# Kernel optimization log

Measured on AMD Instinct MI355X. Metric: run time of the kernel, lower is better.

Reference implementation:

```python
import jax, jax.numpy as jnp
import numpy as np
from jax import lax

B, S, F, H, O, U = 512, 168, 12, 128, 3, 256
PERIODS = (3, 6, 12, 24)


def _glorot(key, shape):
    fan_in = shape[-1]
    fan_out = shape[-2] if len(shape) >= 2 else shape[-1]
    scale = jnp.sqrt(2.0 / (fan_in + fan_out))
    return jax.random.normal(key, shape, jnp.float32) * scale


def setup_inputs() -> dict:
    key = jax.random.key(0)
    ks = iter(jax.random.split(key, 64))
    inp = {"x": jax.random.normal(next(ks), (B, 1, F, S), jnp.float32)}
    # 3 SFF groups (group1: enc_in=12, groups 2/3: enc_in=3) share conv/linear shapes per period
    for p in PERIODS:
        k = 1 + 2 * (p // 2)
        inp[f"conv{p}"] = _glorot(next(ks), (3, k))             # [group, kernel]
        inp[f"lin{p}"] = _glorot(next(ks), (3, S // p, S // p))  # [group, seg_y, seg_x]
    inp["Wb0"] = _glorot(next(ks), (U, F + H)); inp["bb0"] = jnp.zeros((U,), jnp.float32)
    inp["Wb1"] = _glorot(next(ks), (U, U));     inp["bb1"] = jnp.zeros((U,), jnp.float32)
    inp["Wff1"] = _glorot(next(ks), (H, U));    inp["bff1"] = jnp.zeros((H,), jnp.float32)
    inp["Wff2"] = _glorot(next(ks), (H, U));    inp["bff2"] = jnp.zeros((H,), jnp.float32)
    inp["Wta"] = _glorot(next(ks), (H, U));     inp["bta"] = jnp.zeros((H,), jnp.float32)
    inp["Wtb"] = _glorot(next(ks), (H, U));     inp["btb"] = jnp.zeros((H,), jnp.float32)
    inp["Wfc"] = _glorot(next(ks), (O, H));     inp["bfc"] = jnp.zeros((O,), jnp.float32)
    inp["Wfits"] = _glorot(next(ks), (O, S, S))  # FF: individual per-channel linear seq->pred
    return inp


def _sff(x, conv_w, lin_w, p):
    # x: [B, S, C]; conv_w: [k]; lin_w: [seg_y, seg_x]
    Bx, Sx, C = x.shape
    xp = jnp.transpose(x, (0, 2, 1))                      # [B, C, S]
    xr = xp.reshape(Bx * C, 1, Sx)
    pad = p // 2
    conv = lax.conv_general_dilated(xr, conv_w.reshape(1, 1, -1), (1,), [(pad, pad)],
                                    dimension_numbers=("NCH", "OIH", "NCH"))
    xc = conv.reshape(Bx, C, Sx) + xp                     # residual smoothing
    seg = Sx // p
    xc = jnp.transpose(xc.reshape(Bx * C, seg, p), (0, 2, 1))  # [B*C, p, seg_x]
    y = jnp.einsum("npk,qk->npq", xc, lin_w)              # [B*C, p, seg_y]
    y = jnp.transpose(y, (0, 2, 1)).reshape(Bx, C, -1)    # [B, C, pred]
    return jnp.transpose(y, (0, 2, 1))                    # [B, pred, C]


def reference(x, conv3, lin3, conv6, lin6, conv12, lin12, conv24, lin24,
              Wb0, bb0, Wb1, bb1, Wff1, bff1, Wff2, bff2,
              Wta, bta, Wtb, btb, Wfc, bfc, Wfits):
    convs = {3: conv3, 6: conv6, 12: conv12, 24: conv24}
    lins = {3: lin3, 6: lin6, 12: lin12, 24: lin24}

    xs = jnp.transpose(x[:, 0], (0, 2, 1))                # [B, S, F]
    seq_mean = jnp.mean(xs, axis=1, keepdims=True)        # [B, 1, F]
    xs = xs - seq_mean

    x1 = sum(_sff(xs, convs[p][0], lins[p][0], p) for p in PERIODS) * 0.25   # [B,S,F]
    xin3 = x1[:, :, :3]
    x2 = sum(_sff(xin3, convs[p][1], lins[p][1], p) for p in PERIODS) * 0.25  # [B,S,3]
    x3 = sum(_sff(xin3, convs[p][2], lins[p][2], p) for p in PERIODS) * 0.25  # [B,S,3]

    # CfC recurrence (ts == 1.0 everywhere; dropout in eval mode = identity)
    def step(h, xt):
        z = jnp.concatenate([xt, h], axis=1)
        z = jax.nn.silu(z @ Wb0.T + bb0)
        z = jax.nn.silu(z @ Wb1.T + bb1)
        ff1 = jnp.tanh(z @ Wff1.T + bff1)
        ff2 = jnp.tanh(z @ Wff2.T + bff2)
        t_interp = jax.nn.sigmoid((z @ Wta.T + bta) + (z @ Wtb.T + btb))
        h_new = ff1 * (1.0 - t_interp) + t_interp * ff2
        return h_new, h_new

    h0 = jnp.zeros((x1.shape[0], Wff1.shape[0]), x1.dtype)
    _, hs = lax.scan(step, h0, jnp.transpose(x1, (1, 0, 2)))  # hs: [S, B, H]

    readout = jnp.einsum("sbh,oh->bso", hs, Wfc) + bfc        # [B, S, O]
    readout = readout + x3
    readout = jnp.einsum("bsc,cps->bpc", readout, Wfits)      # FF (per-channel S -> pred)
    return readout + seq_mean[:, :, :3] + x2
```

## Files before the change

### kernel.cpp

```cpp
#include <hip/hip_runtime.h>

#define BB 512
#define SS 168
#define FF 12
#define HH 128
#define UU 256

typedef unsigned short u16;
typedef unsigned int   u32;
typedef _Float16 f16x8 __attribute__((ext_vector_type(8)));
typedef float    f32x4 __attribute__((ext_vector_type(4)));

__device__ __forceinline__ float sigmoidf_(float x){ return __fdividef(1.f, 1.f + __expf(-x)); }
__device__ __forceinline__ float siluf_(float x){ return x * sigmoidf_(x); }
__device__ __forceinline__ float tanhf_(float x){
    float t = __expf(-2.f * fabsf(x));
    float y = __fdividef(1.f - t, 1.f + t);
    return copysignf(y, x);
}
__device__ __forceinline__ u16 f2h_(float v){ return __builtin_bit_cast(u16, (_Float16)v); }
__device__ __forceinline__ f16x8 bc8_(uint4 v){ return __builtin_bit_cast(f16x8, v); }
__device__ __forceinline__ int aslot_(int row, int k){
    return (k >> 5) * 512 + ((k & 31) >> 3) * 128 + row * 8 + (k & 7);
}

#define MFMA16(a, b, acc) __builtin_amdgcn_mfma_f32_16x16x32_f16((a), (b), (acc), 0, 0, 0)

__global__ void prep_kernel(const float* __restrict__ Wb0, const float* __restrict__ Wb1,
                            const float* __restrict__ Wff1, const float* __restrict__ Wff2,
                            const float* __restrict__ Wta, const float* __restrict__ Wtb,
                            const float* __restrict__ Wfc,
                            u16* __restrict__ W0f, u16* __restrict__ W1f, u16* __restrict__ W4f)
{
    int t = blockIdx.x * blockDim.x + threadIdx.x;
    if (t < 43520) {
        int e = t & 7, c = (t >> 3) & 15, g = (t >> 7) & 3, rest = t >> 9;
        int s = rest % 5, tt = rest / 5;
        int k = s * 32 + g * 8 + e;
        float v;
        if (tt < 16) { int u = tt * 16 + c; v = (k < 140) ? Wb0[u * 140 + k] : 0.f; }
        else         { v = (c < 3 && k >= 12 && k < 140) ? Wfc[c * 128 + (k - 12)] : 0.f; }
        W0f[t] = f2h_(v);
    } else if (t < 43520 + 65536) {
        int t1 = t - 43520;
        int e = t1 & 7, c = (t1 >> 3) & 15, g = (t1 >> 7) & 3, rest = t1 >> 9;
        int s = rest & 7, tt = rest >> 3;
        int u = tt * 16 + c, k = s * 32 + g * 8 + e;
        W1f[t1] = f2h_(Wb1[u * 256 + k]);
    } else if (t < 43520 + 65536 + 98304) {
        int t2 = t - 109056;
        int e = t2 & 7, c = (t2 >> 3) & 15, g = (t2 >> 7) & 3, rest = t2 >> 9;
        int s = rest & 7, tt = rest >> 3;
        int u = (tt & 7) * 16 + c, k = s * 32 + g * 8 + e;
        float v;
        if      (tt < 8)  v = Wff1[u * 256 + k];
        else if (tt < 16) v = Wff2[u * 256 + k];
        else              v = Wta[u * 256 + k] + Wtb[u * 256 + k];
        W4f[t2] = f2h_(v);
    }
}

__global__ __launch_bounds__(256) void sffA_kernel(
    const float* __restrict__ x,
    const float* __restrict__ c3,  const float* __restrict__ l3,
    const float* __restrict__ c6,  const float* __restrict__ l6,
    const float* __restrict__ c12, const float* __restrict__ l12,
    const float* __restrict__ c24, const float* __restrict__ l24,
    float* __restrict__ meanbuf, float* __restrict__ x1)
{
    int bc = blockIdx.x;
    int b = bc / FF, c = bc % FF;
    __shared__ float v[SS], cv[SS], red[256];
    int tid = threadIdx.x;

    float raw = 0.f;
    if (tid < SS) raw = x[(b * FF + c) * SS + tid];
    red[tid] = raw;
    __syncthreads();
    for (int off = 128; off > 0; off >>= 1) {
        if (tid < off) red[tid] += red[tid + off];
        __syncthreads();
    }
    float mv = red[0] * (1.f / SS);
    if (tid == 0) meanbuf[b * FF + c] = mv;
    if (tid < SS) v[tid] = raw - mv;
    __syncthreads();

    const float* cw[4]  = {c3, c6, c12, c24};
    const float* lwv[4] = {l3, l6, l12, l24};
    const int P[4] = {3, 6, 12, 24};
    float acc = 0.f;
    for (int pi = 0; pi < 4; ++pi) {
        int p = P[pi], pad = p >> 1, k = 1 + 2 * pad, seg = SS / p;
        const float* cwp = cw[pi];
        float cc = 0.f;
        if (tid < SS) {
            cc = v[tid];
            for (int j = 0; j < k; ++j) {
                int t = tid + j - pad;
                if (t >= 0 && t < SS) cc += cwp[j] * v[t];
            }
        }
        __syncthreads();
        if (tid < SS) cv[tid] = cc;
        __syncthreads();
        if (tid < SS) {
            int q = tid / p, ph = tid - q * p;
            const float* lwp = lwv[pi];
            float a = 0.f;
            for (int kk = 0; kk < seg; ++kk) a += lwp[q * seg + kk] * cv[kk * p + ph];
            acc += a;
        }
    }
    if (tid < SS) x1[(b * SS + tid) * FF + c] = 0.25f * acc;
}

__global__ __launch_bounds__(256) void sffB_kernel(
    const float* __restrict__ x1,
    const float* __restrict__ c3,  const float* __restrict__ l3,
    const float* __restrict__ c6,  const float* __restrict__ l6,
    const float* __restrict__ c12, const float* __restrict__ l12,
    const float* __restrict__ c24, const float* __restrict__ l24,
    float* __restrict__ x2, float* __restrict__ x3)
{
    int bc = blockIdx.x;
    int b = bc / 3, c = bc % 3;
    __shared__ float v[SS], cv[SS];
    int tid = threadIdx.x;
    float raw = 0.f;
    if (tid < SS) raw = x1[(b * SS + tid) * FF + c];
    if (tid < SS) v[tid] = raw;
    __syncthreads();

    const float* cw[4]  = {c3, c6, c12, c24};
    const float* lwv[4] = {l3, l6, l12, l24};
    const int P[4] = {3, 6, 12, 24};
    float acc2 = 0.f, acc3 = 0.f;
    for (int pi = 0; pi < 4; ++pi) {
        int p = P[pi], pad = p >> 1, k = 1 + 2 * pad, seg = SS / p;
        for (int row = 1; row <= 2; ++row) {
            const float* cwp = cw[pi] + row * k;
            float cc = 0.f;
            if (tid < SS) {
                cc = v[tid];
                for (int j = 0; j < k; ++j) {
                    int t = tid + j - pad;
                    if (t >= 0 && t < SS) cc += cwp[j] * v[t];
                }
            }
            __syncthreads();
            if (tid < SS) cv[tid] = cc;
            __syncthreads();
            if (tid < SS) {
                int q = tid / p, ph = tid - q * p;
                const float* lwp = lwv[pi] + row * seg * seg;
                float a = 0.f;
                for (int kk = 0; kk < seg; ++kk) a += lwp[q * seg + kk] * cv[kk * p + ph];
                if (row == 1) acc2 += a; else acc3 += a;
            }
        }
    }
    if (tid < SS) {
        x2[(b * SS + tid) * 3 + c] = 0.25f * acc2;
        x3[(b * SS + tid) * 3 + c] = 0.25f * acc3;
    }
}

__global__ __launch_bounds__(512, 2) void scan_kernel(
    const float* __restrict__ x1g,
    const uint4* __restrict__ W0f, const uint4* __restrict__ W1f, const uint4* __restrict__ W4f,
    const float* __restrict__ bb0, const float* __restrict__ bb1,
    const float* __restrict__ bff1, const float* __restrict__ bff2,
    const float* __restrict__ bta,  const float* __restrict__ btb,
    const float* __restrict__ bfc,
    float* __restrict__ r1g)
{
    const int b0 = blockIdx.x * 8;
    const int tid = threadIdx.x;
    const int w = tid >> 6, lane = tid & 63;
    const int cl = lane & 15, grp = lane >> 4;

    __shared__ __align__(16) u16 W0ro_s[2560];
    __shared__ __align__(16) u16 xh[16128];
    __shared__ __align__(16) u16 zin_s[2560];
    __shared__ __align__(16) u16 z1_s[4096];
    __shared__ __align__(16) u16 z2_s[4096];
    __shared__ __align__(16) float r1s[4032];
    __shared__ float bfcs[4];

    uint4* W0ro4 = (uint4*)W0ro_s;
    uint4* zin4  = (uint4*)zin_s;
    uint4* z1_4  = (uint4*)z1_s;
    uint4* z2_4  = (uint4*)z2_s;

    f16x8 w0a[5], w0b[5];
    f16x8 w1f0[8], w1f1[8], w4a[8], w4b[8], w4c[8];
    #pragma unroll
    for (int s = 0; s < 5; ++s) {
        w0a[s] = bc8_(W0f[((w    ) * 5 + s) * 64 + lane]);
        w0b[s] = bc8_(W0f[((w + 8) * 5 + s) * 64 + lane]);
    }
    #pragma unroll
    for (int s = 0; s < 8; ++s) {
        w1f0[s] = bc8_(W1f[((w     ) * 8 + s) * 64 + lane]);
        w1f1[s] = bc8_(W1f[((w +  8) * 8 + s) * 64 + lane]);
        w4a[s]  = bc8_(W4f[((w     ) * 8 + s) * 64 + lane]);
        w4b[s]  = bc8_(W4f[((w +  8) * 8 + s) * 64 + lane]);
        w4c[s]  = bc8_(W4f[((w + 16) * 8 + s) * 64 + lane]);
    }
    const int u = w * 16 + cl;
    const float bz1a = bb0[u],  bz1b = bb0[128 + u];
    const float bz2a = bb1[u],  bz2b = bb1[128 + u];
    const float bf1r = bff1[u], bf2r = bff2[u];
    const float btsr = bta[u] + btb[u];

    for (int i = tid; i < 320; i += 512) W0ro4[i] = W0f[5120 + i];
    for (int i = tid; i < 16128; i += 512) {
        int s = i / 96, rem = i - s * 96, r = rem / 12, ii = rem - r * 12;
        xh[i] = f2h_(x1g[((b0 + r) * SS + s) * FF + ii]);
    }
    for (int i = tid; i < 320; i += 512) zin4[i] = make_uint4(0, 0, 0, 0);
    for (int i = tid; i < 512; i += 512) z1_4[i] = make_uint4(0, 0, 0, 0);
    for (int i = tid; i < 512; i += 512) z2_4[i] = make_uint4(0, 0, 0, 0);
    if (tid < 3) bfcs[tid] = bfc[tid];
    __syncthreads();
    if (tid < 96) {
        int r = tid / 12, i = tid % 12;
        int trow = (r >> 1) * 4 + (r & 1);
        zin_s[aslot_(trow, i)] = xh[tid];
    }
    __syncthreads();

    #pragma unroll 1
    for (int s = 0; s < SS; ++s) {
        f32x4 a1a0 = {0.f,0.f,0.f,0.f}, a1a1 = {0.f,0.f,0.f,0.f};
        f32x4 a1b0 = {0.f,0.f,0.f,0.f}, a1b1 = {0.f,0.f,0.f,0.f};
        f32x4 accr = {0.f,0.f,0.f,0.f};
        #pragma unroll
        for (int ks = 0; ks < 5; ++ks) {
            f16x8 av = bc8_(zin4[ks * 64 + lane]);
            if (ks & 1) { a1a1 = MFMA16(av, w0a[ks], a1a1); a1b1 = MFMA16(av, w0b[ks], a1b1); }
            else        { a1a0 = MFMA16(av, w0a[ks], a1a0); a1b0 = MFMA16(av, w0b[ks], a1b0); }
            if (w == 0) accr = MFMA16(av, bc8_(W0ro4[ks * 64 + lane]), accr);
        }
        if (w == 0 && s > 0 && cl < 3) {
            r1s[(2 * grp    ) * 504 + (s - 1) * 3 + cl] = accr[0] + bfcs[cl];
            r1s[(2 * grp + 1) * 504 + (s - 1) * 3 + cl] = accr[1] + bfcs[cl];
        }

        {
            int t0r = grp * 4, t1r = grp * 4 + 1;
            z1_s[aslot_(t0r, u)]       = f2h_(siluf_(a1a0[0] + a1a1[0] + bz1a));
            z1_s[aslot_(t1r, u)]       = f2h_(siluf_(a1a0[1] + a1a1[1] + bz1a));
            z1_s[aslot_(t0r, 128 + u)] = f2h_(siluf_(a1b0[0] + a1b1[0] + bz1b));
            z1_s[aslot_(t1r, 128 + u)] = f2h_(siluf_(a1b0[1] + a1b1[1] + bz1b));
        }
        __syncthreads();

        f32x4 a2a0 = {0.f,0.f,0.f,0.f}, a2a1 = {0.f,0.f,0.f,0.f};
        f32x4 a2b0 = {0.f,0.f,0.f,0.f}, a2b1 = {0.f,0.f,0.f,0.f};
        #pragma unroll
        for (int ks = 0; ks < 8; ++ks) {
            f16x8 av = bc8_(z1_4[ks * 64 + lane]);
            if (ks & 1) { a2a1 = MFMA16(av, w1f0[ks], a2a1); a2b1 = MFMA16(av, w1f1[ks], a2b1); }
            else        { a2a0 = MFMA16(av, w1f0[ks], a2a0); a2b0 = MFMA16(av, w1f1[ks], a2b0); }
        }
        {
            int t0r = grp * 4, t1r = grp * 4 + 1;
            z2_s[aslot_(t0r, u)]       = f2h_(siluf_(a2a0[0] + a2a1[0] + bz2a));
            z2_s[aslot_(t1r, u)]       = f2h_(siluf_(a2a0[1] + a2a1[1] + bz2a));
            z2_s[aslot_(t0r, 128 + u)] = f2h_(siluf_(a2b0[0] + a2b1[0] + bz2b));
            z2_s[aslot_(t1r, 128 + u)] = f2h_(siluf_(a2b0[1] + a2b1[1] + bz2b));
        }
        __syncthreads();

        f32x4 c3a0 = {0.f,0.f,0.f,0.f}, c3a1 = {0.f,0.f,0.f,0.f};
        f32x4 c3b0 = {0.f,0.f,0.f,0.f}, c3b1 = {0.f,0.f,0.f,0.f};
        f32x4 c3c0 = {0.f,0.f,0.f,0.f}, c3c1 = {0.f,0.f,0.f,0.f};
        #pragma unroll
        for (int ks = 0; ks < 8; ++ks) {
            f16x8 av = bc8_(z2_4[ks * 64 + lane]);
            if (ks & 1) {
                c3a1 = MFMA16(av, w4a[ks], c3a1);
                c3b1 = MFMA16(av, w4b[ks], c3b1);
                c3c1 = MFMA16(av, w4c[ks], c3c1);
            } else {
                c3a0 = MFMA16(av, w4a[ks], c3a0);
                c3b0 = MFMA16(av, w4b[ks], c3b0);
                c3c0 = MFMA16(av, w4c[ks], c3c0);
            }
        }

        #pragma unroll
        for (int q = 0; q < 2; ++q) {
            float ff1v = tanhf_(c3a0[q] + c3a1[q] + bf1r);
            float ff2v = tanhf_(c3b0[q] + c3b1[q] + bf2r);
            float tv   = sigmoidf_(c3c0[q] + c3c1[q] + btsr);
            float h    = ff1v + tv * (ff2v - ff1v);
            zin_s[aslot_(grp * 4 + q, 12 + u)] = f2h_(h);
        }
        if (tid >= 416 && s + 1 < SS) {
            int idx = tid - 416;
            int r = idx / 12, i = idx % 12;
            int trow = (r >> 1) * 4 + (r & 1);
            zin_s[aslot_(trow, i)] = xh[(s + 1) * 96 + idx];
        }
        __syncthreads();
    }

    if (w == 0) {
        f32x4 accr = {0.f, 0.f, 0.f, 0.f};
        #pragma unroll
        for (int ks = 0; ks < 5; ++ks)
            accr = MFMA16(bc8_(zin4[ks * 64 + lane]),
                          bc8_(W0ro4[ks * 64 + lane]), accr);
        if (cl < 3) {
            r1s[(2 * grp    ) * 504 + 167 * 3 + cl] = accr[0] + bfcs[cl];
            r1s[(2 * grp + 1) * 504 + 167 * 3 + cl] = accr[1] + bfcs[cl];
        }
    }
    __syncthreads();
    for (int idx = tid; idx < 4032; idx += 512) {
        int r = idx / 504, rem = idx - r * 504;
        r1g[(b0 + r) * 504 + rem] = r1s[r * 504 + rem];
    }
}

__global__ __launch_bounds__(256) void fits_kernel(
    const float* __restrict__ r1, const float* __restrict__ x3,
    const float* __restrict__ Wfits,
    const float* __restrict__ x2, const float* __restrict__ meanbuf,
    float* __restrict__ out)
{
    int bid = blockIdx.x;
    int bt = bid & 7;
    int rest = bid >> 3;
    int c = rest % 3;
    int pt = rest / 3;
    int b0 = bt * 64, p0 = pt * 28;
    __shared__ float rT[168][65];
    __shared__ float wT[28][168];
    int t = threadIdx.x;
    for (int idx = t; idx < 64 * 168; idx += 256) {
        int b = idx / 168, s = idx - b * 168;
        int gi = ((b0 + b) * 168 + s) * 3 + c;
        rT[s][b] = r1[gi] + x3[gi];
    }
    for (int idx = t; idx < 28 * 168; idx += 256) {
        int p = idx / 168, s = idx - p * 168;
        wT[p][s] = Wfits[(c * 168 + p0 + p) * 168 + s];
    }
    __syncthreads();
    int b = t & 63, pq = t >> 6;
    float acc[7] = {0, 0, 0, 0, 0, 0, 0};
    for (int s = 0; s < 168; ++s) {
        float v = rT[s][b];
        #pragma unroll
        for (int j = 0; j < 7; ++j) acc[j] += v * wT[pq * 7 + j][s];
    }
    float mb = meanbuf[(b0 + b) * 12 + c];
    #pragma unroll
    for (int j = 0; j < 7; ++j) {
        int p = p0 + pq * 7 + j;
        int gi = ((b0 + b) * 168 + p) * 3 + c;
        out[gi] = acc[j] + mb + x2[gi];
    }
}

extern "C" void kernel_launch(void* const* d_in, const int* in_sizes, int n_in,
                              void* d_out, int out_size, void* d_ws, size_t ws_size,
                              hipStream_t stream) {
    const float* x    = (const float*)d_in[0];
    const float* c3   = (const float*)d_in[1];
    const float* l3   = (const float*)d_in[2];
    const float* c6   = (const float*)d_in[3];
    const float* l6   = (const float*)d_in[4];
    const float* c12  = (const float*)d_in[5];
    const float* l12  = (const float*)d_in[6];
    const float* c24  = (const float*)d_in[7];
    const float* l24  = (const float*)d_in[8];
    const float* Wb0  = (const float*)d_in[9];
    const float* bb0  = (const float*)d_in[10];
    const float* Wb1  = (const float*)d_in[11];
    const float* bb1  = (const float*)d_in[12];
    const float* Wff1 = (const float*)d_in[13];
    const float* bff1 = (const float*)d_in[14];
    const float* Wff2 = (const float*)d_in[15];
    const float* bff2 = (const float*)d_in[16];
    const float* Wta  = (const float*)d_in[17];
    const float* bta  = (const float*)d_in[18];
    const float* Wtb  = (const float*)d_in[19];
    const float* btb  = (const float*)d_in[20];
    const float* Wfc  = (const float*)d_in[21];
    const float* bfc  = (const float*)d_in[22];
    const float* Wfits= (const float*)d_in[23];

    float* ws      = (float*)d_ws;
    float* meanbuf = ws;
    float* x1      = meanbuf + 6144;
    float* x2      = x1 + 1032192;
    float* x3      = x2 + 258048;
    float* r1      = x3 + 258048;
    u16*   W0f     = (u16*)(r1 + 258048);
    u16*   W1f     = W0f + 43520;
    u16*   W4f     = W1f + 65536;
    float* out     = (float*)d_out;

    prep_kernel<<<(207360 + 255) / 256, 256, 0, stream>>>(Wb0, Wb1, Wff1, Wff2, Wta, Wtb, Wfc, W0f, W1f, W4f);
    sffA_kernel<<<BB * FF, 256, 0, stream>>>(x, c3, l3, c6, l6, c12, l12, c24, l24, meanbuf, x1);
    sffB_kernel<<<BB * 3, 256, 0, stream>>>(x1, c3, l3, c6, l6, c12, l12, c24, l24, x2, x3);
    scan_kernel<<<BB / 8, 512, 0, stream>>>(x1,
                                            (const uint4*)W0f, (const uint4*)W1f, (const uint4*)W4f,
                                            bb0, bb1, bff1, bff2, bta, btb, bfc, r1);
    fits_kernel<<<144, 256, 0, stream>>>(r1, x3, Wfits, x2, meanbuf, out);
}
```

Measured before the change: 413.1 us.

## Fuse prep and SFF kernels into one front kernel; halve batch per scan block

The weight-prep, sffA and sffB kernels are merged into a single front kernel. Prep work runs in dedicated blocks, and the channel blocks for c<3 go on to compute the x2/x3 SFF stage from their own x1 values, which removes two launches and the x1 re-read. The scan kernel now handles 4 batch rows per block instead of 8, using only row 0 of each 4-row MFMA group, so twice as many blocks run the serial recurrence. Each block now does less useful work per MFMA, in exchange for more parallelism across CUs.

Result: faster. 342.2 us (-17.2%).

```diff
diff --git a/kernel.cpp b/kernel.cpp
--- a/kernel.cpp
+++ b/kernel.cpp
@@ -26,49 +26,54 @@
 
 #define MFMA16(a, b, acc) __builtin_amdgcn_mfma_f32_16x16x32_f16((a), (b), (acc), 0, 0, 0)
 
-__global__ void prep_kernel(const float* __restrict__ Wb0, const float* __restrict__ Wb1,
-                            const float* __restrict__ Wff1, const float* __restrict__ Wff2,
-                            const float* __restrict__ Wta, const float* __restrict__ Wtb,
-                            const float* __restrict__ Wfc,
-                            u16* __restrict__ W0f, u16* __restrict__ W1f, u16* __restrict__ W4f)
-{
-    int t = blockIdx.x * blockDim.x + threadIdx.x;
-    if (t < 43520) {
-        int e = t & 7, c = (t >> 3) & 15, g = (t >> 7) & 3, rest = t >> 9;
-        int s = rest % 5, tt = rest / 5;
-        int k = s * 32 + g * 8 + e;
-        float v;
-        if (tt < 16) { int u = tt * 16 + c; v = (k < 140) ? Wb0[u * 140 + k] : 0.f; }
-        else         { v = (c < 3 && k >= 12 && k < 140) ? Wfc[c * 128 + (k - 12)] : 0.f; }
-        W0f[t] = f2h_(v);
-    } else if (t < 43520 + 65536) {
-        int t1 = t - 43520;
-        int e = t1 & 7, c = (t1 >> 3) & 15, g = (t1 >> 7) & 3, rest = t1 >> 9;
-        int s = rest & 7, tt = rest >> 3;
-        int u = tt * 16 + c, k = s * 32 + g * 8 + e;
-        W1f[t1] = f2h_(Wb1[u * 256 + k]);
-    } else if (t < 43520 + 65536 + 98304) {
-        int t2 = t - 109056;
-        int e = t2 & 7, c = (t2 >> 3) & 15, g = (t2 >> 7) & 3, rest = t2 >> 9;
-        int s = rest & 7, tt = rest >> 3;
-        int u = (tt & 7) * 16 + c, k = s * 32 + g * 8 + e;
-        float v;
-        if      (tt < 8)  v = Wff1[u * 256 + k];
-        else if (tt < 16) v = Wff2[u * 256 + k];
-        else              v = Wta[u * 256 + k] + Wtb[u * 256 + k];
-        W4f[t2] = f2h_(v);
-    }
-}
-
-__global__ __launch_bounds__(256) void sffA_kernel(
+#define PREP_BLOCKS 810
+#define SFFA_BLOCKS (BB * FF)
+
+__global__ __launch_bounds__(256) void front_kernel(
     const float* __restrict__ x,
     const float* __restrict__ c3,  const float* __restrict__ l3,
     const float* __restrict__ c6,  const float* __restrict__ l6,
     const float* __restrict__ c12, const float* __restrict__ l12,
     const float* __restrict__ c24, const float* __restrict__ l24,
-    float* __restrict__ meanbuf, float* __restrict__ x1)
+    const float* __restrict__ Wb0, const float* __restrict__ Wb1,
+    const float* __restrict__ Wff1, const float* __restrict__ Wff2,
+    const float* __restrict__ Wta, const float* __restrict__ Wtb,
+    const float* __restrict__ Wfc,
+    u16* __restrict__ W0f, u16* __restrict__ W1f, u16* __restrict__ W4f,
+    float* __restrict__ meanbuf, float* __restrict__ x1,
+    float* __restrict__ x2, float* __restrict__ x3)
 {
-    int bc = blockIdx.x;
+    if (blockIdx.x < PREP_BLOCKS) {
+        int t = blockIdx.x * 256 + threadIdx.x;
+        if (t < 43520) {
+            int e = t & 7, c = (t >> 3) & 15, g = (t >> 7) & 3, rest = t >> 9;
+            int s = rest % 5, tt = rest / 5;
+            int k = s * 32 + g * 8 + e;
+            float v;
+            if (tt < 16) { int u = tt * 16 + c; v = (k < 140) ? Wb0[u * 140 + k] : 0.f; }
+            else         { v = (c < 3 && k >= 12 && k < 140) ? Wfc[c * 128 + (k - 12)] : 0.f; }
+            W0f[t] = f2h_(v);
+        } else if (t < 43520 + 65536) {
+            int t1 = t - 43520;
+            int e = t1 & 7, c = (t1 >> 3) & 15, g = (t1 >> 7) & 3, rest = t1 >> 9;
+            int s = rest & 7, tt = rest >> 3;
+            int u = tt * 16 + c, k = s * 32 + g * 8 + e;
+            W1f[t1] = f2h_(Wb1[u * 256 + k]);
+        } else if (t < 43520 + 65536 + 98304) {
+            int t2 = t - 109056;
+            int e = t2 & 7, c = (t2 >> 3) & 15, g = (t2 >> 7) & 3, rest = t2 >> 9;
+            int s = rest & 7, tt = rest >> 3;
+            int u = (tt & 7) * 16 + c, k = s * 32 + g * 8 + e;
+            float v;
+            if      (tt < 8)  v = Wff1[u * 256 + k];
+            else if (tt < 16) v = Wff2[u * 256 + k];
+            else              v = Wta[u * 256 + k] + Wtb[u * 256 + k];
+            W4f[t2] = f2h_(v);
+        }
+        return;
+    }
+
+    int bc = blockIdx.x - PREP_BLOCKS;
     int b = bc / FF, c = bc % FF;
     __shared__ float v[SS], cv[SS], red[256];
     int tid = threadIdx.x;
@@ -112,29 +117,13 @@
             acc += a;
         }
     }
-    if (tid < SS) x1[(b * SS + tid) * FF + c] = 0.25f * acc;
-}
-
-__global__ __launch_bounds__(256) void sffB_kernel(
-    const float* __restrict__ x1,
-    const float* __restrict__ c3,  const float* __restrict__ l3,
-    const float* __restrict__ c6,  const float* __restrict__ l6,
-    const float* __restrict__ c12, const float* __restrict__ l12,
-    const float* __restrict__ c24, const float* __restrict__ l24,
-    float* __restrict__ x2, float* __restrict__ x3)
-{
-    int bc = blockIdx.x;
-    int b = bc / 3, c = bc % 3;
-    __shared__ float v[SS], cv[SS];
-    int tid = threadIdx.x;
-    float raw = 0.f;
-    if (tid < SS) raw = x1[(b * SS + tid) * FF + c];
-    if (tid < SS) v[tid] = raw;
-    __syncthreads();
-
-    const float* cw[4]  = {c3, c6, c12, c24};
-    const float* lwv[4] = {l3, l6, l12, l24};
-    const int P[4] = {3, 6, 12, 24};
+    float x1v = 0.25f * acc;
+    if (tid < SS) x1[(b * SS + tid) * FF + c] = x1v;
+    if (c >= 3) return;
+
+    __syncthreads();
+    if (tid < SS) v[tid] = x1v;
+    __syncthreads();
     float acc2 = 0.f, acc3 = 0.f;
     for (int pi = 0; pi < 4; ++pi) {
         int p = P[pi], pad = p >> 1, k = 1 + 2 * pad, seg = SS / p;
@@ -175,17 +164,17 @@
     const float* __restrict__ bfc,
     float* __restrict__ r1g)
 {
-    const int b0 = blockIdx.x * 8;
+    const int b0 = blockIdx.x * 4;
     const int tid = threadIdx.x;
     const int w = tid >> 6, lane = tid & 63;
     const int cl = lane & 15, grp = lane >> 4;
 
     __shared__ __align__(16) u16 W0ro_s[2560];
-    __shared__ __align__(16) u16 xh[16128];
+    __shared__ __align__(16) u16 xh[8064];
     __shared__ __align__(16) u16 zin_s[2560];
     __shared__ __align__(16) u16 z1_s[4096];
     __shared__ __align__(16) u16 z2_s[4096];
-    __shared__ __align__(16) float r1s[4032];
+    __shared__ __align__(16) float r1s[2016];
     __shared__ float bfcs[4];
 
     uint4* W0ro4 = (uint4*)W0ro_s;
@@ -215,8 +204,8 @@
     const float btsr = bta[u] + btb[u];
 
     for (int i = tid; i < 320; i += 512) W0ro4[i] = W0f[5120 + i];
-    for (int i = tid; i < 16128; i += 512) {
-        int s = i / 96, rem = i - s * 96, r = rem / 12, ii = rem - r * 12;
+    for (int i = tid; i < 8064; i += 512) {
+        int s = i / 48, rem = i - s * 48, r = rem / 12, ii = rem - r * 12;
         xh[i] = f2h_(x1g[((b0 + r) * SS + s) * FF + ii]);
     }
     for (int i = tid; i < 320; i += 512) zin4[i] = make_uint4(0, 0, 0, 0);
@@ -224,10 +213,9 @@
     for (int i = tid; i < 512; i += 512) z2_4[i] = make_uint4(0, 0, 0, 0);
     if (tid < 3) bfcs[tid] = bfc[tid];
     __syncthreads();
-    if (tid < 96) {
+    if (tid < 48) {
         int r = tid / 12, i = tid % 12;
-        int trow = (r >> 1) * 4 + (r & 1);
-        zin_s[aslot_(trow, i)] = xh[tid];
+        zin_s[aslot_(r * 4, i)] = xh[tid];
     }
     __syncthreads();
 
@@ -243,17 +231,13 @@
             else        { a1a0 = MFMA16(av, w0a[ks], a1a0); a1b0 = MFMA16(av, w0b[ks], a1b0); }
             if (w == 0) accr = MFMA16(av, bc8_(W0ro4[ks * 64 + lane]), accr);
         }
-        if (w == 0 && s > 0 && cl < 3) {
-            r1s[(2 * grp    ) * 504 + (s - 1) * 3 + cl] = accr[0] + bfcs[cl];
-            r1s[(2 * grp + 1) * 504 + (s - 1) * 3 + cl] = accr[1] + bfcs[cl];
-        }
+        if (w == 0 && s > 0 && cl < 3)
+            r1s[grp * 504 + (s - 1) * 3 + cl] = accr[0] + bfcs[cl];
 
         {
-            int t0r = grp * 4, t1r = grp * 4 + 1;
-            z1_s[aslot_(t0r, u)]       = f2h_(siluf_(a1a0[0] + a1a1[0] + bz1a));
-            z1_s[aslot_(t1r, u)]       = f2h_(siluf_(a1a0[1] + a1a1[1] + bz1a));
-            z1_s[aslot_(t0r, 128 + u)] = f2h_(siluf_(a1b0[0] + a1b1[0] + bz1b));
-            z1_s[aslot_(t1r, 128 + u)] = f2h_(siluf_(a1b0[1] + a1b1[1] + bz1b));
+            int tr = grp * 4;
+            z1_s[aslot_(tr, u)]       = f2h_(siluf_(a1a0[0] + a1a1[0] + bz1a));
+            z1_s[aslot_(tr, 128 + u)] = f2h_(siluf_(a1b0[0] + a1b1[0] + bz1b));
         }
         __syncthreads();
 
@@ -266,11 +250,9 @@
             else        { a2a0 = MFMA16(av, w1f0[ks], a2a0); a2b0 = MFMA16(av, w1f1[ks], a2b0); }
         }
         {
-            int t0r = grp * 4, t1r = grp * 4 + 1;
-            z2_s[aslot_(t0r, u)]       = f2h_(siluf_(a2a0[0] + a2a1[0] + bz2a));
-            z2_s[aslot_(t1r, u)]       = f2h_(siluf_(a2a0[1] + a2a1[1] + bz2a));
-            z2_s[aslot_(t0r, 128 + u)] = f2h_(siluf_(a2b0[0] + a2b1[0] + bz2b));
-            z2_s[aslot_(t1r, 128 + u)] = f2h_(siluf_(a2b0[1] + a2b1[1] + bz2b));
+            int tr = grp * 4;
+            z2_s[aslot_(tr, u)]       = f2h_(siluf_(a2a0[0] + a2a1[0] + bz2a));
+            z2_s[aslot_(tr, 128 + u)] = f2h_(siluf_(a2b0[0] + a2b1[0] + bz2b));
         }
         __syncthreads();
 
@@ -291,19 +273,17 @@
             }
         }
 
-        #pragma unroll
-        for (int q = 0; q < 2; ++q) {
-            float ff1v = tanhf_(c3a0[q] + c3a1[q] + bf1r);
-            float ff2v = tanhf_(c3b0[q] + c3b1[q] + bf2r);
-            float tv   = sigmoidf_(c3c0[q] + c3c1[q] + btsr);
+        {
+            float ff1v = tanhf_(c3a0[0] + c3a1[0] + bf1r);
+            float ff2v = tanhf_(c3b0[0] + c3b1[0] + bf2r);
+            float tv   = sigmoidf_(c3c0[0] + c3c1[0] + btsr);
             float h    = ff1v + tv * (ff2v - ff1v);
-            zin_s[aslot_(grp * 4 + q, 12 + u)] = f2h_(h);
-        }
-        if (tid >= 416 && s + 1 < SS) {
-            int idx = tid - 416;
+            zin_s[aslot_(grp * 4, 12 + u)] = f2h_(h);
+        }
+        if (tid >= 448 && tid < 496 && s + 1 < SS) {
+            int idx = tid - 448;
             int r = idx / 12, i = idx % 12;
-            int trow = (r >> 1) * 4 + (r & 1);
-            zin_s[aslot_(trow, i)] = xh[(s + 1) * 96 + idx];
+            zin_s[aslot_(r * 4, i)] = xh[(s + 1) * 48 + idx];
         }
         __syncthreads();
     }
@@ -314,13 +294,11 @@
         for (int ks = 0; ks < 5; ++ks)
             accr = MFMA16(bc8_(zin4[ks * 64 + lane]),
                           bc8_(W0ro4[ks * 64 + lane]), accr);
-        if (cl < 3) {
-            r1s[(2 * grp    ) * 504 + 167 * 3 + cl] = accr[0] + bfcs[cl];
-            r1s[(2 * grp + 1) * 504 + 167 * 3 + cl] = accr[1] + bfcs[cl];
-        }
-    }
-    __syncthreads();
-    for (int idx = tid; idx < 4032; idx += 512) {
+        if (cl < 3)
+            r1s[grp * 504 + 167 * 3 + cl] = accr[0] + bfcs[cl];
+    }
+    __syncthreads();
+    for (int idx = tid; idx < 2016; idx += 512) {
         int r = idx / 504, rem = idx - r * 504;
         r1g[(b0 + r) * 504 + rem] = r1s[r * 504 + rem];
     }
@@ -406,10 +384,11 @@
     u16*   W4f     = W1f + 65536;
     float* out     = (float*)d_out;
 
-    prep_kernel<<<(207360 + 255) / 256, 256, 0, stream>>>(Wb0, Wb1, Wff1, Wff2, Wta, Wtb, Wfc, W0f, W1f, W4f);
-    sffA_kernel<<<BB * FF, 256, 0, stream>>>(x, c3, l3, c6, l6, c12, l12, c24, l24, meanbuf, x1);
-    sffB_kernel<<<BB * 3, 256, 0, stream>>>(x1, c3, l3, c6, l6, c12, l12, c24, l24, x2, x3);
-    scan_kernel<<<BB / 8, 512, 0, stream>>>(x1,
+    front_kernel<<<PREP_BLOCKS + SFFA_BLOCKS, 256, 0, stream>>>(
+        x, c3, l3, c6, l6, c12, l12, c24, l24,
+        Wb0, Wb1, Wff1, Wff2, Wta, Wtb, Wfc,
+        W0f, W1f, W4f, meanbuf, x1, x2, x3);
+    scan_kernel<<<BB / 4, 512, 0, stream>>>(x1,
                                             (const uint4*)W0f, (const uint4*)W1f, (const uint4*)W4f,
                                             bb0, bb1, bff1, bff2, bta, btb, bfc, r1);
     fits_kernel<<<144, 256, 0, stream>>>(r1, x3, Wfits, x2, meanbuf, out);
```
